# Optimization experiments

Hardware: AMD Instinct MI355X
Metric: run time of the kernel (lower is better)

The kernel has to match this reference:

```python
import jax, jax.numpy as jnp
import numpy as np
from jax import lax

B, T_ENC, T_DEC, H = 512, 64, 18, 128
NF = 17  # input_size - 1 (column 14 is dropped)
COLS = np.array(list(range(14)) + list(range(15, 18)))


def _lstm_cell(x, h, c, Wih, Whh, bih, bhh):
    # PyTorch LSTMCell: gates = x@Wih^T + bih + h@Whh^T + bhh, order i,f,g,o
    g = x @ Wih.T + bih + h @ Whh.T + bhh
    i, f, gg, o = jnp.split(g, 4, axis=-1)
    c2 = jax.nn.sigmoid(f) * c + jax.nn.sigmoid(i) * jnp.tanh(gg)
    h2 = jax.nn.sigmoid(o) * jnp.tanh(c2)
    return h2, c2


def setup_inputs() -> dict:
    key = jax.random.key(0)
    ks = jax.random.split(key, 32)
    s = 0.08
    def w(k, shape):
        return jax.random.normal(k, shape, jnp.float32) * s
    return {
        "input_p_q": jax.random.normal(ks[0], (B, T_ENC, 18), jnp.float32),
        "label_p": jax.random.normal(ks[1], (B, T_ENC), jnp.float32),
        "Wih1": w(ks[2], (4 * H, NF)), "Whh1": w(ks[3], (4 * H, H)),
        "bih1": w(ks[4], (4 * H,)), "bhh1": w(ks[5], (4 * H,)),
        "Wih2": w(ks[6], (4 * H, H + 1)), "Whh2": w(ks[7], (4 * H, H)),
        "bih2": w(ks[8], (4 * H,)), "bhh2": w(ks[9], (4 * H,)),
        "Wihd": w(ks[10], (4 * H, H)), "Whhd": w(ks[11], (4 * H, H)),
        "bihd": w(ks[12], (4 * H,)), "bhhd": w(ks[13], (4 * H,)),
        "Wi_w": w(ks[14], (T_ENC, T_ENC)), "Wi_b": w(ks[15], (T_ENC,)),
        "We_w": w(ks[16], (T_ENC, 2 * H)),
        "Vd_w": w(ks[17], (1, T_ENC)), "Vd_b": w(ks[18], (1,)),
        "Wi2_w": w(ks[19], (T_ENC, T_ENC)), "Wi2_b": w(ks[20], (T_ENC,)),
        "We2_w": w(ks[21], (T_ENC, 2 * H)),
        "Vd2_w": w(ks[22], (1, T_ENC)), "Vd2_b": w(ks[23], (1,)),
        "Wx_w": w(ks[24], (H, H)), "Wx_b": w(ks[25], (H,)),
        "Wh_w": w(ks[26], (H, 2 * H)),
        "V_w": w(ks[27], (1, H)), "V_b": w(ks[28], (1,)),
        "reg_w": w(ks[29], (1, H)), "reg_b": w(ks[30], (1,)),
    }


def reference(input_p_q, label_p, Wih1, Whh1, bih1, bhh1, Wih2, Whh2, bih2, bhh2,
              Wihd, Whhd, bihd, bhhd, Wi_w, Wi_b, We_w, Vd_w, Vd_b,
              Wi2_w, Wi2_b, We2_w, Vd2_w, Vd2_b, Wx_w, Wx_b, Wh_w, V_w, V_b,
              reg_w, reg_b):
    B_ = input_p_q.shape[0]
    inputs = input_p_q[:, :T_ENC, COLS]  # [B, T, 17]
    z = jnp.zeros((B_, H), input_p_q.dtype)

    # stage 1: per-step spatial attention over the 17 driving series + LSTM encoder
    WiX = jnp.swapaxes(inputs, 1, 2) @ Wi_w.T + Wi_b  # [B, 17, T] (step-invariant)
    def step1(carry, x_t):
        h, c = carry
        e = jnp.concatenate([h, c], axis=-1) @ We_w.T  # [B, T]
        score = jnp.tanh(WiX + e[:, None, :]) @ Vd_w[0] + Vd_b[0]  # [B, 17]
        a = jax.nn.softmax(score, axis=1)
        h, c = _lstm_cell(x_t * a, h, c, Wih1, Whh1, bih1, bhh1)
        return (h, c), h
    _, mid = lax.scan(step1, (z, z), jnp.swapaxes(inputs, 0, 1))
    mid = jnp.swapaxes(mid, 0, 1)  # [B, T, H]
    mid2 = jnp.concatenate([mid, label_p[:, :T_ENC, None]], axis=2)  # [B, T, H+1]

    # stage 2: spatial attention over H+1 channels + second LSTM encoder
    Wi2X = jnp.swapaxes(mid2, 1, 2) @ Wi2_w.T + Wi2_b  # [B, H+1, T]
    def step2(carry, x_t):
        h, c = carry
        e = jnp.concatenate([h, c], axis=-1) @ We2_w.T  # [B, T]
        score = jnp.tanh(Wi2X + e[:, None, :]) @ Vd2_w[0] + Vd2_b[0]  # [B, H+1]
        a = jax.nn.softmax(score, axis=1)
        h, c = _lstm_cell(x_t * a, h, c, Wih2, Whh2, bih2, bhh2)
        return (h, c), h
    _, final = lax.scan(step2, (z, z), jnp.swapaxes(mid2, 0, 1))
    final = jnp.swapaxes(final, 0, 1)  # [B, T, H]

    # stage 3: temporal attention decoder for T_DEC + 6 steps
    WxF = final @ Wx_w.T + Wx_b  # [B, T, H] (step-invariant)
    def step3(carry, _):
        h, c = carry
        e = jnp.concatenate([h, c], axis=-1) @ Wh_w.T  # [B, H]
        s = jnp.tanh(WxF + e[:, None, :]) @ V_w[0] + V_b[0]  # [B, T]
        a = jax.nn.softmax(s, axis=1)
        din = jnp.einsum('bt,bth->bh', a, final)  # context vector
        h, c = _lstm_cell(din, h, c, Wihd, Whhd, bihd, bhhd)
        return (h, c), h
    _, dec = lax.scan(step3, (z, z), None, length=T_DEC + 6)
    dec = jnp.swapaxes(dec, 0, 1)  # [B, T_DEC+6, H]
    out = dec @ reg_w[0] + reg_b[0]  # [B, T_DEC+6]
    return out[:, -T_DEC:]
```

## Files before the change

kernel.cpp:

```cpp
#include <hip/hip_runtime.h>
#include <hip/hip_fp16.h>

#define TENC 64
#define TDEC 18
#define NDEC 24
#define NF1  17
#define NF2  129
#define HH   128

#define OFF_WI   0
#define OFF_WI2  4096
#define U_GB   8192
#define U_GDH  45568
#define U_GDX  78336
#define U_GFH  111616
#define U_GFX  144384
#define U_WE   177152
#define U_WE2  185344
#define U_WH   193536
#define U_WXH  209920

#define SB   68
#define SWF  132
#define XIN  1200
#define BIGN 8772

typedef _Float16 h2t __attribute__((ext_vector_type(2)));

#if defined(__has_builtin)
#if __has_builtin(__builtin_amdgcn_fdot2)
#define HAVE_FDOT2 1
#endif
#endif

template<int I> struct ic_t { static constexpr int v = I; };
template<int N, typename F>
__device__ __forceinline__ void sfor(F&& f)
{
    if constexpr (N > 0) { sfor<N - 1>((F&&)f); f(ic_t<N - 1>{}); }
}

__device__ __forceinline__ float fdot2p(unsigned w, unsigned x, float acc)
{
    h2t hw = __builtin_bit_cast(h2t, w);
    h2t hx = __builtin_bit_cast(h2t, x);
#ifdef HAVE_FDOT2
    return __builtin_amdgcn_fdot2(hw, hx, acc, false);
#else
    return acc + (float)hw.x * (float)hx.x + (float)hw.y * (float)hx.y;
#endif
}

__device__ __forceinline__ unsigned pkh_d(float a, float b)
{
    __half ha = __float2half(a), hb = __float2half(b);
    return (unsigned)__half_as_ushort(ha) | ((unsigned)__half_as_ushort(hb) << 16);
}

__device__ __forceinline__ float hget(unsigned u, int hi)
{
    h2t v = __builtin_bit_cast(h2t, u);
    return hi ? (float)v.y : (float)v.x;
}

__device__ __forceinline__ float fsig(float x) { return 1.f / (1.f + __expf(-x)); }
__device__ __forceinline__ float ftanh(float x)
{
    x = fminf(fmaxf(x, -15.f), 15.f);
    float e = __expf(2.f * x);
    return (e - 1.f) / (e + 1.f);
}

__global__ void pack_f2(const float* Wi, const float* Wi2, float* ws)
{
    const int m = blockIdx.y;
    const float* src = m ? Wi2 : Wi;
    const int off = m ? OFF_WI2 : OFF_WI;
    const int G = 64, K = 64, n = G * K;
    for (int i = blockIdx.x * blockDim.x + threadIdx.x; i < n; i += gridDim.x * blockDim.x) {
        int q = i & 3, gk = i >> 2;
        int kk = gk / G, g = gk - kk * G;
        ws[off + i] = src[g * K + kk * 4 + q];
    }
}

__global__ void pack_gp(const float* Wih, const float* Whh, int Kx, int KXP, int qbase,
                        unsigned base, int ldg, unsigned* wsu)
{
    const int g = threadIdx.x;
    const int q = qbase + blockIdx.x;
    int k0 = 2 * q, k1 = 2 * q + 1;
    float f0 = (k0 < KXP) ? ((k0 < Kx) ? Wih[g * Kx + k0] : 0.f) : Whh[g * HH + (k0 - KXP)];
    float f1 = (k1 < KXP) ? ((k1 < Kx) ? Wih[g * Kx + k1] : 0.f) : Whh[g * HH + (k1 - KXP)];
    wsu[base + (unsigned)blockIdx.x * (unsigned)ldg + g] = pkh_d(f0, f1);
}

__global__ void pack_ew(const float* W, int J, int nPQ, int nI, unsigned base, unsigned* wsu)
{
    int idx = blockIdx.x * blockDim.x + threadIdx.x;
    if (idx >= J * 128) return;
    int j = idx >> 7, r = idx & 127;
    int pq = r / nI, i = r - pq * nI;
    int pr = i * nPQ + pq;
    wsu[base + idx] = pkh_d(W[j * 256 + 2 * pr], W[j * 256 + 2 * pr + 1]);
}

__global__ __launch_bounds__(512, 2)
void dstp_main(const float* __restrict__ inq, const float* __restrict__ labp,
               const float* __restrict__ bih1, const float* __restrict__ bhh1,
               const float* __restrict__ bih2, const float* __restrict__ bhh2,
               const float* __restrict__ bihd, const float* __restrict__ bhhd,
               const float* __restrict__ Wi_b, const float* __restrict__ Vd_w, const float* __restrict__ Vd_b,
               const float* __restrict__ Wi2_b, const float* __restrict__ Vd2_w, const float* __restrict__ Vd2_b,
               const float* __restrict__ Wx_b, const float* __restrict__ V_w, const float* __restrict__ V_b,
               const float* __restrict__ reg_w, const float* __restrict__ reg_b,
               const float* __restrict__ ws, float* __restrict__ out)
{
    __shared__ __align__(16) unsigned buf_h[2][TENC][64];
    __shared__ __align__(16) float big[2][BIGN];
    __shared__ __align__(16) unsigned hcp[2][128];
    __shared__ __align__(16) unsigned xhp[2][132];
    __shared__ __align__(16) float ebuf[2][128];
    __shared__ float sc[2][132];
    __shared__ float att[2][64];
    __shared__ float pre[2][512];
    __shared__ float lab[2][64];
    __shared__ __align__(16) float vw1[64], vw2[64], vwf[128], rw[128];
    __shared__ float rsm[4];

    const int tid  = threadIdx.x;
    const int b0   = blockIdx.x * 2;
    const unsigned* wsu = (const unsigned*)ws;
    const float4* Wip  = (const float4*)(ws + OFF_WI);
    const float4* Wi2p = (const float4*)(ws + OFF_WI2);

    const float bg1 = bih1[tid] + bhh1[tid];
    const float bg2 = bih2[tid] + bhh2[tid];
    const float bgd = bihd[tid] + bhhd[tid];
    float creg = 0.f;

    if (tid < 128) lab[tid >> 6][tid & 63] = labp[(b0 + (tid >> 6)) * TENC + (tid & 63)];
    if (tid < 64)        vw1[tid]       = Vd_w[tid];
    else if (tid < 128)  vw2[tid - 64]  = Vd2_w[tid - 64];
    else if (tid < 256)  vwf[tid - 128] = V_w[tid - 128];
    else if (tid < 384)  rw[tid - 256]  = reg_w[tid - 256];
    for (int i = tid; i < 2176; i += 512) {
        int bb = i / 1088, r = i - bb * 1088, t = r / NF1, f = r - t * NF1;
        big[bb][XIN + r] = inq[((b0 + bb) * TENC + t) * 18 + f + (f >= 14)];
    }
    __syncthreads();
    for (int i = tid; i < 2176; i += 512) {
        int bb = i / 1088, r = i - bb * 1088, f = r >> 6, j = r & 63;
        float acc = Wi_b[j];
        for (int tt = 0; tt < 16; ++tt) {
            float4 w = Wip[tt * 64 + j];
            acc += big[bb][XIN + (4 * tt + 0) * NF1 + f] * w.x
                 + big[bb][XIN + (4 * tt + 1) * NF1 + f] * w.y
                 + big[bb][XIN + (4 * tt + 2) * NF1 + f] * w.z
                 + big[bb][XIN + (4 * tt + 3) * NF1 + f] * w.w;
        }
        big[bb][f * SB + j] = acc;
    }

    {
        if (tid < 256) hcp[tid >> 7][tid & 127] = 0u;
        if (tid < 264) xhp[tid / 132][tid % 132] = 0u;
        creg = 0.f;
        unsigned wB[73];
        sfor<73>([&](auto I) { wB[I.v] = wsu[U_GB + I.v * 512 + tid]; });
        unsigned we[16];
        const int ewb = U_WE + ((tid >> 3) << 7) + ((tid & 7) << 4);
        sfor<16>([&](auto I) { we[I.v] = wsu[ewb + I.v]; });
        __syncthreads();

        for (int t = 0; t < TENC; ++t) {
            {
                int j = tid >> 3, pq = tid & 7;
                float a0 = 0.f, a1 = 0.f, b0c = 0.f, b1c = 0.f;
                sfor<8>([&](auto I) {
                    a0  = fdot2p(we[I.v], hcp[0][I.v * 8 + pq], a0);
                    a1  = fdot2p(we[I.v], hcp[1][I.v * 8 + pq], a1);
                    b0c = fdot2p(we[8 + I.v], hcp[0][(8 + I.v) * 8 + pq], b0c);
                    b1c = fdot2p(we[8 + I.v], hcp[1][(8 + I.v) * 8 + pq], b1c);
                });
                float s0 = a0 + b0c, s1 = a1 + b1c;
                s0 += __shfl_xor(s0, 1, 8); s1 += __shfl_xor(s1, 1, 8);
                s0 += __shfl_xor(s0, 2, 8); s1 += __shfl_xor(s1, 2, 8);
                s0 += __shfl_xor(s0, 4, 8); s1 += __shfl_xor(s1, 4, 8);
                if (pq == 0) { ebuf[0][j] = s0; ebuf[1][j] = s1; }
            }
            __syncthreads();
            for (int i = tid; i < 544; i += 512) {
                int bb = i / 272, r = i - bb * 272, f = r >> 4, pp = r & 15;
                float4 wx = *(const float4*)&big[bb][f * SB + pp * 4];
                float4 e4 = *(const float4*)&ebuf[bb][pp * 4];
                float4 v4 = *(const float4*)&vw1[pp * 4];
                float acc = ftanh(wx.x + e4.x) * v4.x + ftanh(wx.y + e4.y) * v4.y
                          + ftanh(wx.z + e4.z) * v4.z + ftanh(wx.w + e4.w) * v4.w;
                acc += __shfl_xor(acc, 1, 16);
                acc += __shfl_xor(acc, 2, 16);
                acc += __shfl_xor(acc, 4, 16);
                acc += __shfl_xor(acc, 8, 16);
                if (pp == 0) sc[bb][f] = acc + Vd_b[0];
            }
            __syncthreads();
            if (tid < 128) {
                int bb = tid >> 6, l = tid & 63;
                float v = (l < NF1) ? sc[bb][l] : -1e30f;
                float m = v;
                for (int d = 32; d; d >>= 1) m = fmaxf(m, __shfl_xor(m, d, 64));
                float e = (l < NF1) ? __expf(v - m) : 0.f;
                float s = e;
                for (int d = 32; d; d >>= 1) s += __shfl_xor(s, d, 64);
                float xv = (l < NF1) ? big[bb][XIN + t * NF1 + l] * (e / s) : 0.f;
                float xp = __shfl_xor(xv, 1, 64);
                if (!(l & 1) && l < 18) xhp[bb][l >> 1] = pkh_d(xv, xp);
            }
            __syncthreads();
            {
                const uint4* x0q = (const uint4*)xhp[0];
                const uint4* x1q = (const uint4*)xhp[1];
                float p00 = bg1, p01 = 0.f, p02 = 0.f, p03 = 0.f;
                float p10 = bg1, p11 = 0.f, p12 = 0.f, p13 = 0.f;
                sfor<18>([&](auto C) {
                    uint4 X0 = x0q[C.v], X1 = x1q[C.v];
                    p00 = fdot2p(wB[4 * C.v + 0], X0.x, p00);
                    p10 = fdot2p(wB[4 * C.v + 0], X1.x, p10);
                    p01 = fdot2p(wB[4 * C.v + 1], X0.y, p01);
                    p11 = fdot2p(wB[4 * C.v + 1], X1.y, p11);
                    p02 = fdot2p(wB[4 * C.v + 2], X0.z, p02);
                    p12 = fdot2p(wB[4 * C.v + 2], X1.z, p12);
                    p03 = fdot2p(wB[4 * C.v + 3], X0.w, p03);
                    p13 = fdot2p(wB[4 * C.v + 3], X1.w, p13);
                });
                p00 = fdot2p(wB[72], xhp[0][72], p00);
                p10 = fdot2p(wB[72], xhp[1][72], p10);
                pre[0][tid] = (p00 + p01) + (p02 + p03);
                pre[1][tid] = (p10 + p11) + (p12 + p13);
            }
            __syncthreads();
            if (tid < 256) {
                int bb = tid >> 7, k = tid & 127;
                float gi = pre[bb][k], gf = pre[bb][128 + k], gg = pre[bb][256 + k], go = pre[bb][384 + k];
                float c2 = fsig(gf) * creg + fsig(gi) * ftanh(gg);
                float h2v = fsig(go) * ftanh(c2);
                creg = c2;
                float hp = __shfl_xor(h2v, 1, 64);
                float cp = __shfl_xor(c2, 1, 64);
                if (!(k & 1)) {
                    unsigned hu = pkh_d(h2v, hp);
                    hcp[bb][k >> 1] = hu;
                    hcp[bb][64 + (k >> 1)] = pkh_d(c2, cp);
                    xhp[bb][9 + (k >> 1)] = hu;
                    buf_h[bb][t][k >> 1] = hu;
                }
            }
            __syncthreads();
        }
    }

    if (tid < 256) hcp[tid >> 7][tid & 127] = 0u;
    if (tid < 264) xhp[tid / 132][tid % 132] = 0u;
    creg = 0.f;
    for (int i = tid; i < 16512; i += 512) {
        int bb = i / 8256, r = i - bb * 8256, f = r >> 6, j = r & 63;
        float acc = Wi2_b[j];
        if (f < HH) {
            int fp = f >> 1, fh = f & 1;
            for (int tt = 0; tt < 16; ++tt) {
                float4 w = Wi2p[tt * 64 + j];
                acc += hget(buf_h[bb][4 * tt + 0][fp], fh) * w.x
                     + hget(buf_h[bb][4 * tt + 1][fp], fh) * w.y
                     + hget(buf_h[bb][4 * tt + 2][fp], fh) * w.z
                     + hget(buf_h[bb][4 * tt + 3][fp], fh) * w.w;
            }
        } else {
            for (int tt = 0; tt < 16; ++tt) {
                float4 w = Wi2p[tt * 64 + j];
                acc += lab[bb][4 * tt] * w.x + lab[bb][4 * tt + 1] * w.y
                     + lab[bb][4 * tt + 2] * w.z + lab[bb][4 * tt + 3] * w.w;
            }
        }
        big[bb][f * SB + j] = acc;
    }

    {
        unsigned wD[129];
        sfor<65>([&](auto I) { wD[I.v] = wsu[U_GDX + I.v * 512 + tid]; });
        sfor<64>([&](auto I) { wD[65 + I.v] = wsu[U_GDH + I.v * 512 + tid]; });
        unsigned wes[16];
        const int ewb2 = U_WE2 + ((tid >> 3) << 7) + ((tid & 7) << 4);
        sfor<16>([&](auto I) { wes[I.v] = wsu[ewb2 + I.v]; });
        __syncthreads();

        for (int t = 0; t < TENC; ++t) {
            {
                int j = tid >> 3, pq = tid & 7;
                float a0 = 0.f, a1 = 0.f, b0c = 0.f, b1c = 0.f;
                sfor<8>([&](auto I) {
                    a0  = fdot2p(wes[I.v], hcp[0][I.v * 8 + pq], a0);
                    a1  = fdot2p(wes[I.v], hcp[1][I.v * 8 + pq], a1);
                    b0c = fdot2p(wes[8 + I.v], hcp[0][(8 + I.v) * 8 + pq], b0c);
                    b1c = fdot2p(wes[8 + I.v], hcp[1][(8 + I.v) * 8 + pq], b1c);
                });
                float s0 = a0 + b0c, s1 = a1 + b1c;
                s0 += __shfl_xor(s0, 1, 8); s1 += __shfl_xor(s1, 1, 8);
                s0 += __shfl_xor(s0, 2, 8); s1 += __shfl_xor(s1, 2, 8);
                s0 += __shfl_xor(s0, 4, 8); s1 += __shfl_xor(s1, 4, 8);
                if (pq == 0) { ebuf[0][j] = s0; ebuf[1][j] = s1; }
            }
            __syncthreads();
            for (int i = tid; i < 1032; i += 512) {
                int bb = i / 516, r = i - bb * 516, f = r >> 2, pp = r & 3;
                float acc = 0.f;
                #pragma unroll
                for (int c = 0; c < 4; ++c) {
                    float4 wx = *(const float4*)&big[bb][f * SB + pp * 16 + c * 4];
                    float4 e4 = *(const float4*)&ebuf[bb][pp * 16 + c * 4];
                    float4 v4 = *(const float4*)&vw2[pp * 16 + c * 4];
                    acc += ftanh(wx.x + e4.x) * v4.x + ftanh(wx.y + e4.y) * v4.y
                         + ftanh(wx.z + e4.z) * v4.z + ftanh(wx.w + e4.w) * v4.w;
                }
                acc += __shfl_xor(acc, 1, 4);
                acc += __shfl_xor(acc, 2, 4);
                if (pp == 0) sc[bb][f] = acc + Vd2_b[0];
            }
            __syncthreads();
            if (tid < 128) {
                int bb = tid >> 6, l = tid & 63;
                float s1 = sc[bb][l], s2 = sc[bb][l + 64];
                float s3 = (l == 0) ? sc[bb][128] : -1e30f;
                float m = fmaxf(fmaxf(s1, s2), s3);
                for (int d = 32; d; d >>= 1) m = fmaxf(m, __shfl_xor(m, d, 64));
                float e1 = __expf(s1 - m), e2 = __expf(s2 - m);
                float e3 = (l == 0) ? __expf(s3 - m) : 0.f;
                float s = e1 + e2 + e3;
                for (int d = 32; d; d >>= 1) s += __shfl_xor(s, d, 64);
                float inv = 1.f / s;
                float v1 = hget(buf_h[bb][t][l >> 1], l & 1) * e1 * inv;
                float v2 = hget(buf_h[bb][t][32 + (l >> 1)], l & 1) * e2 * inv;
                float v1p = __shfl_xor(v1, 1, 64);
                float v2p = __shfl_xor(v2, 1, 64);
                if (!(l & 1)) {
                    xhp[bb][l >> 1] = pkh_d(v1, v1p);
                    xhp[bb][32 + (l >> 1)] = pkh_d(v2, v2p);
                }
                if (l == 0) xhp[bb][64] = pkh_d(lab[bb][t] * e3 * inv, 0.f);
            }
            __syncthreads();
            {
                const uint4* x0q = (const uint4*)xhp[0];
                const uint4* x1q = (const uint4*)xhp[1];
                float p00 = bg2, p01 = 0.f, p02 = 0.f, p03 = 0.f;
                float p10 = bg2, p11 = 0.f, p12 = 0.f, p13 = 0.f;
                sfor<32>([&](auto C) {
                    uint4 X0 = x0q[C.v], X1 = x1q[C.v];
                    p00 = fdot2p(wD[4 * C.v + 0], X0.x, p00);
                    p10 = fdot2p(wD[4 * C.v + 0], X1.x, p10);
                    p01 = fdot2p(wD[4 * C.v + 1], X0.y, p01);
                    p11 = fdot2p(wD[4 * C.v + 1], X1.y, p11);
                    p02 = fdot2p(wD[4 * C.v + 2], X0.z, p02);
                    p12 = fdot2p(wD[4 * C.v + 2], X1.z, p12);
                    p03 = fdot2p(wD[4 * C.v + 3], X0.w, p03);
                    p13 = fdot2p(wD[4 * C.v + 3], X1.w, p13);
                });
                p00 = fdot2p(wD[128], xhp[0][128], p00);
                p10 = fdot2p(wD[128], xhp[1][128], p10);
                pre[0][tid] = (p00 + p01) + (p02 + p03);
                pre[1][tid] = (p10 + p11) + (p12 + p13);
            }
            __syncthreads();
            if (tid < 256) {
                int bb = tid >> 7, k = tid & 127;
                float gi = pre[bb][k], gf = pre[bb][128 + k], gg = pre[bb][256 + k], go = pre[bb][384 + k];
                float c2 = fsig(gf) * creg + fsig(gi) * ftanh(gg);
                float h2v = fsig(go) * ftanh(c2);
                creg = c2;
                float hp = __shfl_xor(h2v, 1, 64);
                float cp = __shfl_xor(c2, 1, 64);
                if (!(k & 1)) {
                    unsigned hu = pkh_d(h2v, hp);
                    hcp[bb][k >> 1] = hu;
                    hcp[bb][64 + (k >> 1)] = pkh_d(c2, cp);
                    xhp[bb][65 + (k >> 1)] = hu;
                    buf_h[bb][t][k >> 1] = hu;
                }
            }
            __syncthreads();
        }
    }

    if (tid < 256) hcp[tid >> 7][tid & 127] = 0u;
    if (tid < 264) xhp[tid / 132][tid % 132] = 0u;
    creg = 0.f;
    {
        const int j = tid & 127;
        unsigned wxh[64];
        sfor<64>([&](auto I) { wxh[I.v] = wsu[U_WXH + I.v * 128 + j]; });
        for (int u = tid >> 7; u < 128; u += 4) {
            int bb = u >> 6, tt = u & 63;
            const uint4* bq = (const uint4*)buf_h[bb][tt];
            float a0 = Wx_b[j], a1 = 0.f, a2 = 0.f, a3 = 0.f;
            sfor<16>([&](auto C) {
                uint4 X = bq[C.v];
                a0 = fdot2p(wxh[4 * C.v + 0], X.x, a0);
                a1 = fdot2p(wxh[4 * C.v + 1], X.y, a1);
                a2 = fdot2p(wxh[4 * C.v + 2], X.z, a2);
                a3 = fdot2p(wxh[4 * C.v + 3], X.w, a3);
            });
            big[bb][tt * SWF + j] = (a0 + a1) + (a2 + a3);
        }
    }

    {
        unsigned wF[128];
        sfor<64>([&](auto I) { wF[I.v] = wsu[U_GFX + I.v * 512 + tid]; });
        sfor<64>([&](auto I) { wF[64 + I.v] = wsu[U_GFH + I.v * 512 + tid]; });
        unsigned wh[32];
        const int whb = U_WH + ((tid >> 2) << 7) + ((tid & 3) << 5);
        sfor<32>([&](auto I) { wh[I.v] = wsu[whb + I.v]; });
        __syncthreads();

        for (int n = 0; n < NDEC; ++n) {
            {
                int j = tid >> 2, pq = tid & 3;
                float a0 = 0.f, a1 = 0.f, b0c = 0.f, b1c = 0.f;
                sfor<16>([&](auto I) {
                    a0  = fdot2p(wh[I.v], hcp[0][I.v * 4 + pq], a0);
                    a1  = fdot2p(wh[I.v], hcp[1][I.v * 4 + pq], a1);
                    b0c = fdot2p(wh[16 + I.v], hcp[0][(16 + I.v) * 4 + pq], b0c);
                    b1c = fdot2p(wh[16 + I.v], hcp[1][(16 + I.v) * 4 + pq], b1c);
                });
                float s0 = a0 + b0c, s1 = a1 + b1c;
                s0 += __shfl_xor(s0, 1, 4); s1 += __shfl_xor(s1, 1, 4);
                s0 += __shfl_xor(s0, 2, 4); s1 += __shfl_xor(s1, 2, 4);
                if (pq == 0) { ebuf[0][j] = s0; ebuf[1][j] = s1; }
            }
            __syncthreads();
            for (int i = tid; i < 1024; i += 512) {
                int bb = i >> 9, r = i & 511, tt = r >> 3, pp = r & 7;
                float acc = 0.f;
                #pragma unroll
                for (int c = 0; c < 4; ++c) {
                    float4 wx = *(const float4*)&big[bb][tt * SWF + pp * 16 + c * 4];
                    float4 e4 = *(const float4*)&ebuf[bb][pp * 16 + c * 4];
                    float4 v4 = *(const float4*)&vwf[pp * 16 + c * 4];
                    acc += ftanh(wx.x + e4.x) * v4.x + ftanh(wx.y + e4.y) * v4.y
                         + ftanh(wx.z + e4.z) * v4.z + ftanh(wx.w + e4.w) * v4.w;
                }
                acc += __shfl_xor(acc, 1, 8);
                acc += __shfl_xor(acc, 2, 8);
                acc += __shfl_xor(acc, 4, 8);
                if (pp == 0) sc[bb][tt] = acc + V_b[0];
            }
            __syncthreads();
            if (tid < 128) {
                int bb = tid >> 6, l = tid & 63;
                float v = sc[bb][l];
                float m = v;
                for (int d = 32; d; d >>= 1) m = fmaxf(m, __shfl_xor(m, d, 64));
                float e = __expf(v - m);
                float s = e;
                for (int d = 32; d; d >>= 1) s += __shfl_xor(s, d, 64);
                att[bb][l] = e / s;
            }
            __syncthreads();
            for (int i = tid; i < 1024; i += 512) {
                int bb = i >> 9, r = i & 511, k = r >> 2, pq = r & 3;
                int kp = k >> 1, kh = k & 1;
                float acc = 0.f;
                #pragma unroll
                for (int u = 0; u < 16; ++u) {
                    int tt = u * 4 + pq;
                    acc += att[bb][tt] * hget(buf_h[bb][tt][kp], kh);
                }
                acc += __shfl_xor(acc, 1, 64);
                acc += __shfl_xor(acc, 2, 64);
                float dp = __shfl_xor(acc, 4, 64);
                if ((r & 7) == 0) xhp[bb][r >> 3] = pkh_d(acc, dp);
            }
            __syncthreads();
            {
                const uint4* x0q = (const uint4*)xhp[0];
                const uint4* x1q = (const uint4*)xhp[1];
                float p00 = bgd, p01 = 0.f, p02 = 0.f, p03 = 0.f;
                float p10 = bgd, p11 = 0.f, p12 = 0.f, p13 = 0.f;
                sfor<32>([&](auto C) {
                    uint4 X0 = x0q[C.v], X1 = x1q[C.v];
                    p00 = fdot2p(wF[4 * C.v + 0], X0.x, p00);
                    p10 = fdot2p(wF[4 * C.v + 0], X1.x, p10);
                    p01 = fdot2p(wF[4 * C.v + 1], X0.y, p01);
                    p11 = fdot2p(wF[4 * C.v + 1], X1.y, p11);
                    p02 = fdot2p(wF[4 * C.v + 2], X0.z, p02);
                    p12 = fdot2p(wF[4 * C.v + 2], X1.z, p12);
                    p03 = fdot2p(wF[4 * C.v + 3], X0.w, p03);
                    p13 = fdot2p(wF[4 * C.v + 3], X1.w, p13);
                });
                pre[0][tid] = (p00 + p01) + (p02 + p03);
                pre[1][tid] = (p10 + p11) + (p12 + p13);
            }
            __syncthreads();
            if (tid < 256) {
                int bb = tid >> 7, k = tid & 127;
                float gi = pre[bb][k], gf = pre[bb][128 + k], gg = pre[bb][256 + k], go = pre[bb][384 + k];
                float c2 = fsig(gf) * creg + fsig(gi) * ftanh(gg);
                float h2v = fsig(go) * ftanh(c2);
                creg = c2;
                float hp = __shfl_xor(h2v, 1, 64);
                float cp = __shfl_xor(c2, 1, 64);
                if (!(k & 1)) {
                    unsigned hu = pkh_d(h2v, hp);
                    hcp[bb][k >> 1] = hu;
                    hcp[bb][64 + (k >> 1)] = pkh_d(c2, cp);
                    xhp[bb][64 + (k >> 1)] = hu;
                }
                if (n >= 6) {
                    float v = h2v * rw[k];
                    for (int d = 32; d; d >>= 1) v += __shfl_xor(v, d, 64);
                    if ((tid & 63) == 0) rsm[tid >> 6] = v;
                }
            }
            __syncthreads();
            if (n >= 6 && tid < 2)
                out[(b0 + tid) * TDEC + (n - 6)] = rsm[tid * 2] + rsm[tid * 2 + 1] + reg_b[0];
        }
    }
}

extern "C" void kernel_launch(void* const* d_in, const int* in_sizes, int n_in,
                              void* d_out, int out_size, void* d_ws, size_t ws_size,
                              hipStream_t stream)
{
    const float* inq   = (const float*)d_in[0];
    const float* labp  = (const float*)d_in[1];
    const float* Wih1  = (const float*)d_in[2];
    const float* Whh1  = (const float*)d_in[3];
    const float* bih1  = (const float*)d_in[4];
    const float* bhh1  = (const float*)d_in[5];
    const float* Wih2  = (const float*)d_in[6];
    const float* Whh2  = (const float*)d_in[7];
    const float* bih2  = (const float*)d_in[8];
    const float* bhh2  = (const float*)d_in[9];
    const float* Wihd  = (const float*)d_in[10];
    const float* Whhd  = (const float*)d_in[11];
    const float* bihd  = (const float*)d_in[12];
    const float* bhhd  = (const float*)d_in[13];
    const float* Wi_w  = (const float*)d_in[14];
    const float* Wi_b  = (const float*)d_in[15];
    const float* We_w  = (const float*)d_in[16];
    const float* Vd_w  = (const float*)d_in[17];
    const float* Vd_b  = (const float*)d_in[18];
    const float* Wi2_w = (const float*)d_in[19];
    const float* Wi2_b = (const float*)d_in[20];
    const float* We2_w = (const float*)d_in[21];
    const float* Vd2_w = (const float*)d_in[22];
    const float* Vd2_b = (const float*)d_in[23];
    const float* Wx_w  = (const float*)d_in[24];
    const float* Wx_b  = (const float*)d_in[25];
    const float* Wh_w  = (const float*)d_in[26];
    const float* V_w   = (const float*)d_in[27];
    const float* V_b   = (const float*)d_in[28];
    const float* reg_w = (const float*)d_in[29];
    const float* reg_b = (const float*)d_in[30];
    float* ws  = (float*)d_ws;
    unsigned* wsu = (unsigned*)d_ws;
    float* out = (float*)d_out;

    pack_f2<<<dim3(16, 2), 256, 0, stream>>>(Wi_w, Wi2_w, ws);
    pack_gp<<<73, 512, 0, stream>>>(Wih1, Whh1, 17, 18, 0, U_GB, 512, wsu);
    pack_gp<<<65, 512, 0, stream>>>(Wih2, Whh2, 129, 130, 0, U_GDX, 512, wsu);
    pack_gp<<<64, 512, 0, stream>>>(Wih2, Whh2, 129, 130, 65, U_GDH, 512, wsu);
    pack_gp<<<64, 512, 0, stream>>>(Wihd, Whhd, 128, 128, 0, U_GFX, 512, wsu);
    pack_gp<<<64, 512, 0, stream>>>(Wihd, Whhd, 128, 128, 64, U_GFH, 512, wsu);
    pack_gp<<<64, 128, 0, stream>>>(Wx_w, Wx_w, 128, 128, 0, U_WXH, 128, wsu);
    pack_ew<<<8, 1024, 0, stream>>>(We_w, 64, 8, 16, U_WE, wsu);
    pack_ew<<<8, 1024, 0, stream>>>(We2_w, 64, 8, 16, U_WE2, wsu);
    pack_ew<<<16, 1024, 0, stream>>>(Wh_w, 128, 4, 32, U_WH, wsu);
    dstp_main<<<256, 512, 0, stream>>>(inq, labp, bih1, bhh1, bih2, bhh2, bihd, bhhd,
                                       Wi_b, Vd_w, Vd_b, Wi2_b, Vd2_w, Vd2_b,
                                       Wx_b, V_w, V_b, reg_w, reg_b, ws, out);
}
```

Measured before the change: 817.7 us.

## Hoist recurrent h·Whh dot products off the critical path in all three LSTM stages

```diff
diff --git a/kernel.cpp b/kernel.cpp
--- a/kernel.cpp
+++ b/kernel.cpp
@@ -190,6 +190,22 @@
                 if (pq == 0) { ebuf[0][j] = s0; ebuf[1][j] = s1; }
             }
             __syncthreads();
+            float q00 = 0.f, q01 = 0.f, q10 = 0.f, q11 = 0.f;
+            {
+                const uint4* h0q = (const uint4*)hcp[0];
+                const uint4* h1q = (const uint4*)hcp[1];
+                sfor<16>([&](auto C) {
+                    uint4 H0 = h0q[C.v], H1 = h1q[C.v];
+                    q00 = fdot2p(wB[9 + 4 * C.v + 0], H0.x, q00);
+                    q10 = fdot2p(wB[9 + 4 * C.v + 0], H1.x, q10);
+                    q01 = fdot2p(wB[9 + 4 * C.v + 1], H0.y, q01);
+                    q11 = fdot2p(wB[9 + 4 * C.v + 1], H1.y, q11);
+                    q00 = fdot2p(wB[9 + 4 * C.v + 2], H0.z, q00);
+                    q10 = fdot2p(wB[9 + 4 * C.v + 2], H1.z, q10);
+                    q01 = fdot2p(wB[9 + 4 * C.v + 3], H0.w, q01);
+                    q11 = fdot2p(wB[9 + 4 * C.v + 3], H1.w, q11);
+                });
+            }
             for (int i = tid; i < 544; i += 512) {
                 int bb = i / 272, r = i - bb * 272, f = r >> 4, pp = r & 15;
                 float4 wx = *(const float4*)&big[bb][f * SB + pp * 4];
@@ -220,23 +236,22 @@
             {
                 const uint4* x0q = (const uint4*)xhp[0];
                 const uint4* x1q = (const uint4*)xhp[1];
-                float p00 = bg1, p01 = 0.f, p02 = 0.f, p03 = 0.f;
-                float p10 = bg1, p11 = 0.f, p12 = 0.f, p13 = 0.f;
-                sfor<18>([&](auto C) {
+                float p00 = bg1, p10 = bg1;
+                sfor<2>([&](auto C) {
                     uint4 X0 = x0q[C.v], X1 = x1q[C.v];
                     p00 = fdot2p(wB[4 * C.v + 0], X0.x, p00);
                     p10 = fdot2p(wB[4 * C.v + 0], X1.x, p10);
-                    p01 = fdot2p(wB[4 * C.v + 1], X0.y, p01);
-                    p11 = fdot2p(wB[4 * C.v + 1], X1.y, p11);
-                    p02 = fdot2p(wB[4 * C.v + 2], X0.z, p02);
-                    p12 = fdot2p(wB[4 * C.v + 2], X1.z, p12);
-                    p03 = fdot2p(wB[4 * C.v + 3], X0.w, p03);
-                    p13 = fdot2p(wB[4 * C.v + 3], X1.w, p13);
-                });
-                p00 = fdot2p(wB[72], xhp[0][72], p00);
-                p10 = fdot2p(wB[72], xhp[1][72], p10);
-                pre[0][tid] = (p00 + p01) + (p02 + p03);
-                pre[1][tid] = (p10 + p11) + (p12 + p13);
+                    q00 = fdot2p(wB[4 * C.v + 1], X0.y, q00);
+                    q10 = fdot2p(wB[4 * C.v + 1], X1.y, q10);
+                    p00 = fdot2p(wB[4 * C.v + 2], X0.z, p00);
+                    p10 = fdot2p(wB[4 * C.v + 2], X1.z, p10);
+                    q00 = fdot2p(wB[4 * C.v + 3], X0.w, q00);
+                    q10 = fdot2p(wB[4 * C.v + 3], X1.w, q10);
+                });
+                p00 = fdot2p(wB[8], xhp[0][8], p00);
+                p10 = fdot2p(wB[8], xhp[1][8], p10);
+                pre[0][tid] = (p00 + q00) + q01;
+                pre[1][tid] = (p10 + q10) + q11;
             }
             __syncthreads();
             if (tid < 256) {
@@ -251,7 +266,6 @@
                     unsigned hu = pkh_d(h2v, hp);
                     hcp[bb][k >> 1] = hu;
                     hcp[bb][64 + (k >> 1)] = pkh_d(c2, cp);
-                    xhp[bb][9 + (k >> 1)] = hu;
                     buf_h[bb][t][k >> 1] = hu;
                 }
             }
@@ -310,6 +324,22 @@
                 if (pq == 0) { ebuf[0][j] = s0; ebuf[1][j] = s1; }
             }
             __syncthreads();
+            float q00 = 0.f, q01 = 0.f, q10 = 0.f, q11 = 0.f;
+            {
+                const uint4* h0q = (const uint4*)hcp[0];
+                const uint4* h1q = (const uint4*)hcp[1];
+                sfor<16>([&](auto C) {
+                    uint4 H0 = h0q[C.v], H1 = h1q[C.v];
+                    q00 = fdot2p(wD[65 + 4 * C.v + 0], H0.x, q00);
+                    q10 = fdot2p(wD[65 + 4 * C.v + 0], H1.x, q10);
+                    q01 = fdot2p(wD[65 + 4 * C.v + 1], H0.y, q01);
+                    q11 = fdot2p(wD[65 + 4 * C.v + 1], H1.y, q11);
+                    q00 = fdot2p(wD[65 + 4 * C.v + 2], H0.z, q00);
+                    q10 = fdot2p(wD[65 + 4 * C.v + 2], H1.z, q10);
+                    q01 = fdot2p(wD[65 + 4 * C.v + 3], H0.w, q01);
+                    q11 = fdot2p(wD[65 + 4 * C.v + 3], H1.w, q11);
+                });
+            }
             for (int i = tid; i < 1032; i += 512) {
                 int bb = i / 516, r = i - bb * 516, f = r >> 2, pp = r & 3;
                 float acc = 0.f;
@@ -351,23 +381,22 @@
             {
                 const uint4* x0q = (const uint4*)xhp[0];
                 const uint4* x1q = (const uint4*)xhp[1];
-                float p00 = bg2, p01 = 0.f, p02 = 0.f, p03 = 0.f;
-                float p10 = bg2, p11 = 0.f, p12 = 0.f, p13 = 0.f;
-                sfor<32>([&](auto C) {
+                float p00 = bg2, p01 = 0.f, p10 = bg2, p11 = 0.f;
+                sfor<16>([&](auto C) {
                     uint4 X0 = x0q[C.v], X1 = x1q[C.v];
                     p00 = fdot2p(wD[4 * C.v + 0], X0.x, p00);
                     p10 = fdot2p(wD[4 * C.v + 0], X1.x, p10);
                     p01 = fdot2p(wD[4 * C.v + 1], X0.y, p01);
                     p11 = fdot2p(wD[4 * C.v + 1], X1.y, p11);
-                    p02 = fdot2p(wD[4 * C.v + 2], X0.z, p02);
-                    p12 = fdot2p(wD[4 * C.v + 2], X1.z, p12);
-                    p03 = fdot2p(wD[4 * C.v + 3], X0.w, p03);
-                    p13 = fdot2p(wD[4 * C.v + 3], X1.w, p13);
-                });
-                p00 = fdot2p(wD[128], xhp[0][128], p00);
-                p10 = fdot2p(wD[128], xhp[1][128], p10);
-                pre[0][tid] = (p00 + p01) + (p02 + p03);
-                pre[1][tid] = (p10 + p11) + (p12 + p13);
+                    p00 = fdot2p(wD[4 * C.v + 2], X0.z, p00);
+                    p10 = fdot2p(wD[4 * C.v + 2], X1.z, p10);
+                    p01 = fdot2p(wD[4 * C.v + 3], X0.w, p01);
+                    p11 = fdot2p(wD[4 * C.v + 3], X1.w, p11);
+                });
+                p00 = fdot2p(wD[64], xhp[0][64], p00);
+                p10 = fdot2p(wD[64], xhp[1][64], p10);
+                pre[0][tid] = (p00 + p01) + (q00 + q01);
+                pre[1][tid] = (p10 + p11) + (q10 + q11);
             }
             __syncthreads();
             if (tid < 256) {
@@ -382,7 +411,6 @@
                     unsigned hu = pkh_d(h2v, hp);
                     hcp[bb][k >> 1] = hu;
                     hcp[bb][64 + (k >> 1)] = pkh_d(c2, cp);
-                    xhp[bb][65 + (k >> 1)] = hu;
                     buf_h[bb][t][k >> 1] = hu;
                 }
             }
@@ -437,6 +465,22 @@
                 if (pq == 0) { ebuf[0][j] = s0; ebuf[1][j] = s1; }
             }
             __syncthreads();
+            float q00 = 0.f, q01 = 0.f, q10 = 0.f, q11 = 0.f;
+            {
+                const uint4* h0q = (const uint4*)hcp[0];
+                const uint4* h1q = (const uint4*)hcp[1];
+                sfor<16>([&](auto C) {
+                    uint4 H0 = h0q[C.v], H1 = h1q[C.v];
+                    q00 = fdot2p(wF[64 + 4 * C.v + 0], H0.x, q00);
+                    q10 = fdot2p(wF[64 + 4 * C.v + 0], H1.x, q10);
+                    q01 = fdot2p(wF[64 + 4 * C.v + 1], H0.y, q01);
+                    q11 = fdot2p(wF[64 + 4 * C.v + 1], H1.y, q11);
+                    q00 = fdot2p(wF[64 + 4 * C.v + 2], H0.z, q00);
+                    q10 = fdot2p(wF[64 + 4 * C.v + 2], H1.z, q10);
+                    q01 = fdot2p(wF[64 + 4 * C.v + 3], H0.w, q01);
+                    q11 = fdot2p(wF[64 + 4 * C.v + 3], H1.w, q11);
+                });
+            }
             for (int i = tid; i < 1024; i += 512) {
                 int bb = i >> 9, r = i & 511, tt = r >> 3, pp = r & 7;
                 float acc = 0.f;
@@ -483,21 +527,20 @@
             {
                 const uint4* x0q = (const uint4*)xhp[0];
                 const uint4* x1q = (const uint4*)xhp[1];
-                float p00 = bgd, p01 = 0.f, p02 = 0.f, p03 = 0.f;
-                float p10 = bgd, p11 = 0.f, p12 = 0.f, p13 = 0.f;
-                sfor<32>([&](auto C) {
+                float p00 = bgd, p01 = 0.f, p10 = bgd, p11 = 0.f;
+                sfor<16>([&](auto C) {
                     uint4 X0 = x0q[C.v], X1 = x1q[C.v];
                     p00 = fdot2p(wF[4 * C.v + 0], X0.x, p00);
                     p10 = fdot2p(wF[4 * C.v + 0], X1.x, p10);
                     p01 = fdot2p(wF[4 * C.v + 1], X0.y, p01);
                     p11 = fdot2p(wF[4 * C.v + 1], X1.y, p11);
-                    p02 = fdot2p(wF[4 * C.v + 2], X0.z, p02);
-                    p12 = fdot2p(wF[4 * C.v + 2], X1.z, p12);
-                    p03 = fdot2p(wF[4 * C.v + 3], X0.w, p03);
-                    p13 = fdot2p(wF[4 * C.v + 3], X1.w, p13);
-                });
-                pre[0][tid] = (p00 + p01) + (p02 + p03);
-                pre[1][tid] = (p10 + p11) + (p12 + p13);
+                    p00 = fdot2p(wF[4 * C.v + 2], X0.z, p00);
+                    p10 = fdot2p(wF[4 * C.v + 2], X1.z, p10);
+                    p01 = fdot2p(wF[4 * C.v + 3], X0.w, p01);
+                    p11 = fdot2p(wF[4 * C.v + 3], X1.w, p11);
+                });
+                pre[0][tid] = (p00 + p01) + (q00 + q01);
+                pre[1][tid] = (p10 + p11) + (q10 + q11);
             }
             __syncthreads();
             if (tid < 256) {
@@ -512,7 +555,6 @@
                     unsigned hu = pkh_d(h2v, hp);
                     hcp[bb][k >> 1] = hu;
                     hcp[bb][64 + (k >> 1)] = pkh_d(c2, cp);
-                    xhp[bb][64 + (k >> 1)] = hu;
                 }
                 if (n >= 6) {
                     float v = h2v * rw[k];
```

Result: slower. 2.261 ms (+176.5%).
